# Kernel tuning notes

Measured on AMD Instinct MI355X. Metric: run time of the kernel, lower is better.

The kernel has to match this reference:

```python
import jax, jax.numpy as jnp
import numpy as np

DIM = 768
NUM_HEADS = 12
HEAD_DIM = DIM // NUM_HEADS
SCALE = HEAD_DIM ** -0.5


def setup_inputs() -> dict:
    key = jax.random.key(0)
    ks = jax.random.split(key, 6)
    B, N, C = 4, 2048, DIM
    x = jax.random.normal(ks[0], (B, N, C), dtype=jnp.float32)
    qkv_weight = jax.random.normal(ks[1], (3 * C, C), dtype=jnp.float32) * (C ** -0.5)
    q_bias = jax.random.normal(ks[2], (C,), dtype=jnp.float32) * 0.02
    v_bias = jax.random.normal(ks[3], (C,), dtype=jnp.float32) * 0.02
    proj_weight = jax.random.normal(ks[4], (C, C), dtype=jnp.float32) * (C ** -0.5)
    proj_bias = jax.random.normal(ks[5], (C,), dtype=jnp.float32) * 0.02
    return {"x": x, "qkv_weight": qkv_weight, "q_bias": q_bias,
            "v_bias": v_bias, "proj_weight": proj_weight, "proj_bias": proj_bias}


def reference(x, qkv_weight, q_bias, v_bias, proj_weight, proj_bias):
    B, N, C = x.shape
    # bias = concat(q_bias, zeros_like(v_bias), v_bias)
    bias = jnp.concatenate([q_bias, jnp.zeros_like(v_bias), v_bias])
    qkv = x @ qkv_weight.T + bias                      # [B, N, 3C]
    qkv = qkv.reshape(B, N, 3, NUM_HEADS, HEAD_DIM)
    q, k, v = jnp.moveaxis(qkv, 2, 0)                  # each [B, N, H, hd]
    q = jnp.transpose(q, (0, 2, 1, 3)) * SCALE         # [B, H, N, hd]
    k = jnp.transpose(k, (0, 2, 1, 3))
    v = jnp.transpose(v, (0, 2, 1, 3))
    attn = jax.nn.softmax(jnp.einsum('bhqd,bhkd->bhqk', q, k), axis=-1)
    out = jnp.einsum('bhqk,bhkd->bhqd', attn, v)       # [B, H, N, hd]
    out = jnp.transpose(out, (0, 2, 1, 3)).reshape(B, N, C)
    return out @ proj_weight.T + proj_bias
```

## Files before the change

### kernel.cpp

```cpp
#include <hip/hip_runtime.h>
#include <cstdint>
#include <cstddef>

typedef _Float16 f16;
typedef _Float16 f16x8 __attribute__((ext_vector_type(8)));
typedef _Float16 f16x4 __attribute__((ext_vector_type(4)));
typedef __fp16 h16x2 __attribute__((ext_vector_type(2)));
typedef float f32x4 __attribute__((ext_vector_type(4)));
typedef float f32x16 __attribute__((ext_vector_type(16)));

#define DIM 768
#define NHEAD 12
#define HD 64
#define BATCH 4
#define SEQ 2048
#define MROWS (BATCH*SEQ)
#define C3 (3*DIM)
#define NBH (BATCH*NHEAD)

__device__ __forceinline__ f32x4 mfma32(f16x8 a, f16x8 b, f32x4 c) {
  return __builtin_amdgcn_mfma_f32_16x16x32_f16(a, b, c, 0, 0, 0);
}
__device__ __forceinline__ f32x16 mfma3232(f16x8 a, f16x8 b, f32x16 c) {
  return __builtin_amdgcn_mfma_f32_32x32x16_f16(a, b, c, 0, 0, 0);
}

__device__ __forceinline__ void gl2lds16(const void* g, void* l) {
  __builtin_amdgcn_global_load_lds(
      (const __attribute__((address_space(1))) void*)g,
      (__attribute__((address_space(3))) void*)l, 16, 0, 0);
}

__global__ __launch_bounds__(256) void k_convert(
    const float* __restrict__ x, const float* __restrict__ wqkv,
    const float* __restrict__ wproj,
    f16* __restrict__ xh, f16* __restrict__ wqh, f16* __restrict__ wph)
{
  const int NX = MROWS*DIM/4, NW = C3*DIM/4;
  int i = blockIdx.x * 256 + threadIdx.x;
  const float4* src; f16* dst; int idx;
  if (i < NX)         { src = (const float4*)x;     dst = xh;  idx = i; }
  else if (i < NX+NW) { src = (const float4*)wqkv;  dst = wqh; idx = i - NX; }
  else                { src = (const float4*)wproj; dst = wph; idx = i - NX - NW; }
  float4 v = src[idx];
  union { f16 h[4]; uint64_t u; } r;
  r.h[0] = (f16)v.x; r.h[1] = (f16)v.y; r.h[2] = (f16)v.z; r.h[3] = (f16)v.w;
  ((uint64_t*)dst)[idx] = r.u;
}

__device__ __forceinline__ void gemm_tile(
    const f16* __restrict__ A, const f16* __restrict__ B,
    int lda, int ldb, int K, int am0, int bn0,
    f16* smem, f32x4 acc[4][4])
{
  f16* sA0 = smem;         f16* sA1 = smem + 4096;
  f16* sB0 = smem + 8192;  f16* sB1 = smem + 12288;
  const int tid = threadIdx.x, wid = tid >> 6;
  const int lane = tid & 63, lane15 = lane & 15, quad = lane >> 4;
  const int wm = wid >> 1, wn = wid & 1;

  auto stage = [&](int k0, f16* sA, f16* sB) {
    #pragma unroll
    for (int i = 0; i < 2; i++) {
      int j = i*256 + tid;
      int row = j >> 2;
      int sc  = (j & 3) ^ ((row >> 1) & 3);
      gl2lds16(A + (size_t)(am0 + row)*lda + k0 + sc*8, sA + (i*256 + wid*64)*8);
      gl2lds16(B + (size_t)(bn0 + row)*ldb + k0 + sc*8, sB + (i*256 + wid*64)*8);
    }
  };

  const int NK = K >> 5;
  stage(0, sA0, sB0);
  for (int kk = 0; kk < NK; kk++) {
    f16* cA = (kk & 1) ? sA1 : sA0;
    f16* cB = (kk & 1) ? sB1 : sB0;
    __syncthreads();
    if (kk + 1 < NK)
      stage((kk + 1) << 5, (kk & 1) ? sA0 : sA1, (kk & 1) ? sB0 : sB1);
    f16x8 af[4], bf[4];
    #pragma unroll
    for (int t = 0; t < 4; t++) {
      int ra = wm*64 + t*16 + lane15;
      af[t] = *(const f16x8*)(cA + ra*32 + ((quad ^ ((ra >> 1) & 3)) << 3));
      int rb = wn*64 + t*16 + lane15;
      bf[t] = *(const f16x8*)(cB + rb*32 + ((quad ^ ((rb >> 1) & 3)) << 3));
    }
    #pragma unroll
    for (int mt = 0; mt < 4; mt++)
      #pragma unroll
      for (int nt = 0; nt < 4; nt++)
        acc[mt][nt] = mfma32(af[mt], bf[nt], acc[mt][nt]);
  }
}

__global__ __launch_bounds__(256, 4) void k_qkv(
    const f16* __restrict__ xh, const f16* __restrict__ wqh,
    const float* __restrict__ q_bias, const float* __restrict__ v_bias,
    f16* __restrict__ Qh, f16* __restrict__ Kh, f16* __restrict__ Vt)
{
  __shared__ f16 smem[16384];
  f32x4 acc[4][4];
  const f32x4 z4 = {0.f, 0.f, 0.f, 0.f};
  #pragma unroll
  for (int a = 0; a < 4; a++)
    #pragma unroll
    for (int b = 0; b < 4; b++) acc[a][b] = z4;

  const int tid = threadIdx.x, wid = tid >> 6, lane = tid & 63;
  const int lane15 = lane & 15, quad = lane >> 4;
  const int wm = wid >> 1, wn = wid & 1;
  const int cblk = blockIdx.x * 128;
  const int mblk = blockIdx.y * 128;
  const int bb = mblk >> 11, nbase = mblk & (SEQ - 1);
  const float QS = 0.125f * 1.4426950408889634f;

  if (cblk < 2*DIM) {
    gemm_tile(wqh, xh, DIM, DIM, DIM, cblk, mblk, smem, acc);
    const bool isQ = (cblk < DIM);
    #pragma unroll
    for (int mt = 0; mt < 4; mt++) {
      int c0 = cblk + wm*64 + mt*16 + quad*4;
      int cr = isQ ? c0 : (c0 - DIM);
      int h = cr >> 6, d0 = cr & 63;
      float4 qb4 = isQ ? *(const float4*)(q_bias + c0) : make_float4(0,0,0,0);
      f16* dst = isQ ? Qh : Kh;
      f16* base = dst + (((size_t)(bb*NHEAD + h)*SEQ + nbase) << 6) + d0;
      #pragma unroll
      for (int nt = 0; nt < 4; nt++) {
        int n = wn*64 + nt*16 + lane15;
        f32x4 v = acc[mt][nt];
        f16x4 hv;
        if (isQ) {
          hv[0] = (f16)((v[0] + qb4.x) * QS); hv[1] = (f16)((v[1] + qb4.y) * QS);
          hv[2] = (f16)((v[2] + qb4.z) * QS); hv[3] = (f16)((v[3] + qb4.w) * QS);
        } else {
          hv[0] = (f16)v[0]; hv[1] = (f16)v[1]; hv[2] = (f16)v[2]; hv[3] = (f16)v[3];
        }
        *(f16x4*)(base + ((size_t)n << 6)) = hv;
      }
    }
  } else {
    gemm_tile(xh, wqh, DIM, DIM, DIM, mblk, cblk, smem, acc);
    #pragma unroll
    for (int nt = 0; nt < 4; nt++) {
      int c = cblk + wn*64 + nt*16 + lane15;
      int c2 = c - 2*DIM;
      int h = c2 >> 6, d = c2 & 63;
      float b = v_bias[c2];
      f16* base = Vt + ((size_t)(bb*NHEAD + h)*HD + d)*SEQ + nbase;
      #pragma unroll
      for (int mt = 0; mt < 4; mt++) {
        int n0 = wm*64 + mt*16 + quad*4;
        f32x4 v = acc[mt][nt];
        f16x4 hv = {(f16)(v[0]+b), (f16)(v[1]+b), (f16)(v[2]+b), (f16)(v[3]+b)};
        *(f16x4*)(base + n0) = hv;
      }
    }
  }
}

#define KVT 128
#define NIT (SEQ/KVT)
__global__ __launch_bounds__(256, 3) void k_attn(
    const f16* __restrict__ Qh, const f16* __restrict__ Kh,
    const f16* __restrict__ Vt, f16* __restrict__ attnh)
{
  __shared__ f16 smem[16384];
  f16* sK0 = smem;
  f16* sK1 = smem + 8192;

  const int tid = threadIdx.x, wid = tid >> 6, lane = tid & 63;
  const int l31 = lane & 31, hi = lane >> 5;

  const int L = blockIdx.x;
  const int xcd = L & 7, kk = L >> 3;
  const int bh = xcd + 8*(kk >> 4);
  const int q0 = (kk & 15) * 128;
  const int qw = q0 + wid*32;

  const f16* Kbh = Kh + (size_t)bh*SEQ*HD;
  const f16* Vbh = Vt + (size_t)bh*HD*SEQ;

  f16x8 qf[4];
  #pragma unroll
  for (int ks = 0; ks < 4; ks++)
    qf[ks] = *(const f16x8*)(Qh + ((size_t)bh*SEQ + qw + l31)*HD + ks*16 + hi*8);

  const f32x16 z16 = {0.f,0.f,0.f,0.f, 0.f,0.f,0.f,0.f,
                      0.f,0.f,0.f,0.f, 0.f,0.f,0.f,0.f};
  f32x16 o0 = z16, o1 = z16, sacc = z16;
  f16x8 one8;
  #pragma unroll
  for (int j = 0; j < 8; j++) one8[j] = (f16)1.f;

  auto stageK = [&](int kv0, f16* sK) {
    #pragma unroll
    for (int i = 0; i < 4; i++) {
      int j = i*256 + tid;
      int row = j >> 3;
      int sc  = (j & 7) ^ (row & 7);
      gl2lds16(Kbh + (size_t)(kv0 + row)*HD + sc*8, sK + (i*256 + wid*64)*8);
    }
  };

  int koff[4];
  #pragma unroll
  for (int ks = 0; ks < 4; ks++)
    koff[ks] = l31*64 + (((2*ks + hi) ^ (l31 & 7)) << 3);

  const f16* vb0 = Vbh + (size_t)l31*SEQ + hi*8;
  const f16* vb1 = Vbh + (size_t)(32 + l31)*SEQ + hi*8;

  const int pidx = (lane ^ 32) << 2;

  stageK(0, sK0);

  for (int it = 0; it < NIT; it++) {
    f16* cK = (it & 1) ? sK1 : sK0;
    __syncthreads();
    if (it + 1 < NIT)
      stageK((it + 1)*KVT, (it & 1) ? sK0 : sK1);

    #pragma unroll
    for (int c = 0; c < 4; c++) {
      const int p = it*KVT + c*32;
      f16x8 va00 = *(const f16x8*)(vb0 + p);
      f16x8 va01 = *(const f16x8*)(vb0 + p + 16);
      f16x8 va10 = *(const f16x8*)(vb1 + p);
      f16x8 va11 = *(const f16x8*)(vb1 + p + 16);

      f32x16 s = z16;
      #pragma unroll
      for (int ks = 0; ks < 4; ks++) {
        f16x8 ka = *(const f16x8*)(cK + c*2048 + koff[ks]);
        s = mfma3232(ka, qf[ks], s);
      }

      unsigned h[8];
      #pragma unroll
      for (int r = 0; r < 8; r++) {
        union { h16x2 p2; unsigned u; } uu;
        uu.p2 = __builtin_amdgcn_cvt_pkrtz(exp2f(s[2*r]), exp2f(s[2*r+1]));
        h[r] = uu.u;
      }
      int X0 = __builtin_amdgcn_ds_bpermute(pidx, (int)h[0]);
      int X1 = __builtin_amdgcn_ds_bpermute(pidx, (int)h[1]);
      int X2 = __builtin_amdgcn_ds_bpermute(pidx, (int)h[2]);
      int X3 = __builtin_amdgcn_ds_bpermute(pidx, (int)h[3]);
      int X4 = __builtin_amdgcn_ds_bpermute(pidx, (int)h[4]);
      int X5 = __builtin_amdgcn_ds_bpermute(pidx, (int)h[5]);
      int X6 = __builtin_amdgcn_ds_bpermute(pidx, (int)h[6]);
      int X7 = __builtin_amdgcn_ds_bpermute(pidx, (int)h[7]);
      union { unsigned w[4]; f16x8 v; } b0u, b1u;
      b0u.w[0] = hi ? (unsigned)X2 : h[0];
      b0u.w[1] = hi ? (unsigned)X3 : h[1];
      b0u.w[2] = hi ? h[2] : (unsigned)X0;
      b0u.w[3] = hi ? h[3] : (unsigned)X1;
      b1u.w[0] = hi ? (unsigned)X6 : h[4];
      b1u.w[1] = hi ? (unsigned)X7 : h[5];
      b1u.w[2] = hi ? h[6] : (unsigned)X4;
      b1u.w[3] = hi ? h[7] : (unsigned)X5;

      sacc = mfma3232(one8, b0u.v, sacc);
      sacc = mfma3232(one8, b1u.v, sacc);
      o0 = mfma3232(va00, b0u.v, o0);
      o0 = mfma3232(va01, b1u.v, o0);
      o1 = mfma3232(va10, b0u.v, o1);
      o1 = mfma3232(va11, b1u.v, o1);
    }
  }

  const float inv = 1.f / sacc[0];

  __syncthreads();
  f16* tb = smem + wid * (32 * 72);
  #pragma unroll
  for (int g = 0; g < 4; g++) {
    f16x4 h0v = {(f16)(o0[4*g+0]*inv), (f16)(o0[4*g+1]*inv),
                 (f16)(o0[4*g+2]*inv), (f16)(o0[4*g+3]*inv)};
    *(f16x4*)(tb + l31*72 + g*8 + hi*4) = h0v;
    f16x4 h1v = {(f16)(o1[4*g+0]*inv), (f16)(o1[4*g+1]*inv),
                 (f16)(o1[4*g+2]*inv), (f16)(o1[4*g+3]*inv)};
    *(f16x4*)(tb + l31*72 + 32 + g*8 + hi*4) = h1v;
  }
  __syncthreads();
  const int b = bh / NHEAD, hh = bh % NHEAD;
  #pragma unroll
  for (int i = 0; i < 4; i++) {
    int row = i*8 + (lane >> 3);
    f16x8 rv = *(const f16x8*)(tb + row*72 + (lane & 7)*8);
    *(f16x8*)(attnh + ((size_t)b*SEQ + qw + row)*DIM + hh*HD + (lane & 7)*8) = rv;
  }
}

__global__ __launch_bounds__(256, 4) void k_proj(
    const f16* __restrict__ ah, const f16* __restrict__ wph,
    const float* __restrict__ pbias, float* __restrict__ out)
{
  __shared__ f16 smem[16384];
  f32x4 acc[4][4];
  const f32x4 z4 = {0.f, 0.f, 0.f, 0.f};
  #pragma unroll
  for (int a = 0; a < 4; a++)
    #pragma unroll
    for (int b = 0; b < 4; b++) acc[a][b] = z4;

  const int cblk = blockIdx.y * 128;
  const int mblk = blockIdx.x * 128;
  gemm_tile(wph, ah, DIM, DIM, DIM, cblk, mblk, smem, acc);

  const int tid = threadIdx.x, wid = tid >> 6, lane = tid & 63;
  const int lane15 = lane & 15, quad = lane >> 4;
  const int wm = wid >> 1, wn = wid & 1;
  #pragma unroll
  for (int mt = 0; mt < 4; mt++) {
    int c0 = cblk + wm*64 + mt*16 + quad*4;
    float4 b4 = *(const float4*)(pbias + c0);
    #pragma unroll
    for (int nt = 0; nt < 4; nt++) {
      int m = mblk + wn*64 + nt*16 + lane15;
      f32x4 v = acc[mt][nt];
      float4 r = make_float4(v[0]+b4.x, v[1]+b4.y, v[2]+b4.z, v[3]+b4.w);
      *(float4*)(out + (size_t)m*DIM + c0) = r;
    }
  }
}

extern "C" void kernel_launch(void* const* d_in, const int* in_sizes, int n_in,
                              void* d_out, int out_size, void* d_ws, size_t ws_size,
                              hipStream_t stream) {
  const float* x    = (const float*)d_in[0];
  const float* wqkv = (const float*)d_in[1];
  const float* qb   = (const float*)d_in[2];
  const float* vb   = (const float*)d_in[3];
  const float* wp   = (const float*)d_in[4];
  const float* pb   = (const float*)d_in[5];
  float* out = (float*)d_out;

  f16* p = (f16*)d_ws;
  f16* xh  = p; p += (size_t)MROWS*DIM;
  f16* wqh = p; p += (size_t)C3*DIM;
  f16* wph = p; p += (size_t)DIM*DIM;
  f16* Qh  = p; p += (size_t)NBH*SEQ*HD;
  f16* Kh  = p; p += (size_t)NBH*SEQ*HD;
  f16* Vt  = p; p += (size_t)NBH*SEQ*HD;
  f16* attnh = xh;

  k_convert<<<8448, 256, 0, stream>>>(x, wqkv, wp, xh, wqh, wph);
  k_qkv<<<dim3(C3/128, MROWS/128), 256, 0, stream>>>(xh, wqh, qb, vb, Qh, Kh, Vt);
  k_attn<<<dim3((SEQ/128)*NBH), 256, 0, stream>>>(Qh, Kh, Vt, attnh);
  k_proj<<<dim3(MROWS/128, DIM/128), 256, 0, stream>>>(attnh, wph, pb, out);
}
```

Before: 251.0 us.

## Permute V loads to match score layout and prefetch V one chunk ahead

Drops the ds_bpermute exchange of exponentiated scores by loading V in a column order (4-element pieces offset by 4*hi) that matches the MFMA accumulator layout directly. V fragments are now double-buffered in registers and the next chunk is loaded while the current one computes, to hide global load latency. exp2f is also replaced by the hardware exp2 builtin. The cost is more register pressure from two V buffers and smaller 8-byte loads instead of 16-byte ones.

Result: slower. 330.9 us (+31.8%).

```diff
diff --git a/kernel.cpp b/kernel.cpp
--- a/kernel.cpp
+++ b/kernel.cpp
@@ -209,11 +209,55 @@
   for (int ks = 0; ks < 4; ks++)
     koff[ks] = l31*64 + (((2*ks + hi) ^ (l31 & 7)) << 3);
 
-  const f16* vb0 = Vbh + (size_t)l31*SEQ + hi*8;
-  const f16* vb1 = Vbh + (size_t)(32 + l31)*SEQ + hi*8;
-
-  const int pidx = (lane ^ 32) << 2;
-
+  const f16* vb0 = Vbh + (size_t)l31*SEQ + 4*hi;
+  const f16* vb1 = Vbh + (size_t)(32 + l31)*SEQ + 4*hi;
+
+  f16x4 vA[8], vB[8];
+  auto loadV = [&](int p, f16x4* vr) {
+    vr[0] = *(const f16x4*)(vb0 + p);
+    vr[1] = *(const f16x4*)(vb0 + p + 8);
+    vr[2] = *(const f16x4*)(vb0 + p + 16);
+    vr[3] = *(const f16x4*)(vb0 + p + 24);
+    vr[4] = *(const f16x4*)(vb1 + p);
+    vr[5] = *(const f16x4*)(vb1 + p + 8);
+    vr[6] = *(const f16x4*)(vb1 + p + 16);
+    vr[7] = *(const f16x4*)(vb1 + p + 24);
+  };
+
+#define CHUNK(VCUR, VNXT, coff, PRE)                                          \
+  do {                                                                        \
+    PRE;                                                                      \
+    f32x16 s = z16;                                                           \
+    _Pragma("unroll")                                                         \
+    for (int ks = 0; ks < 4; ks++) {                                          \
+      f16x8 ka = *(const f16x8*)(cK + (coff)*2048 + koff[ks]);                \
+      s = mfma3232(ka, qf[ks], s);                                            \
+    }                                                                         \
+    unsigned h[8];                                                            \
+    _Pragma("unroll")                                                         \
+    for (int r = 0; r < 8; r++) {                                             \
+      union { h16x2 p2; unsigned u; } uu;                                     \
+      uu.p2 = __builtin_amdgcn_cvt_pkrtz(__builtin_amdgcn_exp2f(s[2*r]),      \
+                                         __builtin_amdgcn_exp2f(s[2*r+1]));   \
+      h[r] = uu.u;                                                            \
+    }                                                                         \
+    union { unsigned w[4]; f16x8 v; } b0u, b1u;                               \
+    b0u.w[0]=h[0]; b0u.w[1]=h[1]; b0u.w[2]=h[2]; b0u.w[3]=h[3];               \
+    b1u.w[0]=h[4]; b1u.w[1]=h[5]; b1u.w[2]=h[6]; b1u.w[3]=h[7];               \
+    union { f16x4 q[2]; f16x8 v; } a00, a01, a10, a11;                        \
+    a00.q[0]=VCUR[0]; a00.q[1]=VCUR[1];                                       \
+    a01.q[0]=VCUR[2]; a01.q[1]=VCUR[3];                                       \
+    a10.q[0]=VCUR[4]; a10.q[1]=VCUR[5];                                       \
+    a11.q[0]=VCUR[6]; a11.q[1]=VCUR[7];                                       \
+    sacc = mfma3232(one8, b0u.v, sacc);                                       \
+    sacc = mfma3232(one8, b1u.v, sacc);                                       \
+    o0 = mfma3232(a00.v, b0u.v, o0);                                          \
+    o0 = mfma3232(a01.v, b1u.v, o0);                                          \
+    o1 = mfma3232(a10.v, b0u.v, o1);                                          \
+    o1 = mfma3232(a11.v, b1u.v, o1);                                          \
+  } while (0)
+
+  loadV(0, vA);
   stageK(0, sK0);
 
   for (int it = 0; it < NIT; it++) {
@@ -221,55 +265,13 @@
     __syncthreads();
     if (it + 1 < NIT)
       stageK((it + 1)*KVT, (it & 1) ? sK0 : sK1);
-
-    #pragma unroll
-    for (int c = 0; c < 4; c++) {
-      const int p = it*KVT + c*32;
-      f16x8 va00 = *(const f16x8*)(vb0 + p);
-      f16x8 va01 = *(const f16x8*)(vb0 + p + 16);
-      f16x8 va10 = *(const f16x8*)(vb1 + p);
-      f16x8 va11 = *(const f16x8*)(vb1 + p + 16);
-
-      f32x16 s = z16;
-      #pragma unroll
-      for (int ks = 0; ks < 4; ks++) {
-        f16x8 ka = *(const f16x8*)(cK + c*2048 + koff[ks]);
-        s = mfma3232(ka, qf[ks], s);
-      }
-
-      unsigned h[8];
-      #pragma unroll
-      for (int r = 0; r < 8; r++) {
-        union { h16x2 p2; unsigned u; } uu;
-        uu.p2 = __builtin_amdgcn_cvt_pkrtz(exp2f(s[2*r]), exp2f(s[2*r+1]));
-        h[r] = uu.u;
-      }
-      int X0 = __builtin_amdgcn_ds_bpermute(pidx, (int)h[0]);
-      int X1 = __builtin_amdgcn_ds_bpermute(pidx, (int)h[1]);
-      int X2 = __builtin_amdgcn_ds_bpermute(pidx, (int)h[2]);
-      int X3 = __builtin_amdgcn_ds_bpermute(pidx, (int)h[3]);
-      int X4 = __builtin_amdgcn_ds_bpermute(pidx, (int)h[4]);
-      int X5 = __builtin_amdgcn_ds_bpermute(pidx, (int)h[5]);
-      int X6 = __builtin_amdgcn_ds_bpermute(pidx, (int)h[6]);
-      int X7 = __builtin_amdgcn_ds_bpermute(pidx, (int)h[7]);
-      union { unsigned w[4]; f16x8 v; } b0u, b1u;
-      b0u.w[0] = hi ? (unsigned)X2 : h[0];
-      b0u.w[1] = hi ? (unsigned)X3 : h[1];
-      b0u.w[2] = hi ? h[2] : (unsigned)X0;
-      b0u.w[3] = hi ? h[3] : (unsigned)X1;
-      b1u.w[0] = hi ? (unsigned)X6 : h[4];
-      b1u.w[1] = hi ? (unsigned)X7 : h[5];
-      b1u.w[2] = hi ? h[6] : (unsigned)X4;
-      b1u.w[3] = hi ? h[7] : (unsigned)X5;
-
-      sacc = mfma3232(one8, b0u.v, sacc);
-      sacc = mfma3232(one8, b1u.v, sacc);
-      o0 = mfma3232(va00, b0u.v, o0);
-      o0 = mfma3232(va01, b1u.v, o0);
-      o1 = mfma3232(va10, b0u.v, o1);
-      o1 = mfma3232(va11, b1u.v, o1);
-    }
-  }
+    const int p0 = it*KVT;
+    CHUNK(vA, vB, 0, loadV(p0 + 32, vB));
+    CHUNK(vB, vA, 1, loadV(p0 + 64, vA));
+    CHUNK(vA, vB, 2, loadV(p0 + 96, vB));
+    CHUNK(vB, vA, 3, if (it + 1 < NIT) loadV(p0 + 128, vA));
+  }
+#undef CHUNK
 
   const float inv = 1.f / sacc[0];
 
```

## Stage V tiles through padded LDS and drop bpermute P-fragment shuffle

Applied to the files above, without the earlier changes.

V tiles are now prefetched into registers one iteration ahead and written into a padded shared-memory buffer. Each wave then reads the V fragments from LDS in an order that matches the MFMA output layout of the exp'd scores, which removes the eight ds_bpermute cross-lane shuffles per chunk. The exp2 call is replaced by the hardware exp2 builtin. The cost is an extra barrier per iteration, about 17KB more LDS per block, which may lower occupancy from the launch-bounds target of 3 blocks, and more LDS traffic.

Result: faster. 220.1 us (-12.3%).

```diff
diff --git a/kernel.cpp b/kernel.cpp
--- a/kernel.cpp
+++ b/kernel.cpp
@@ -166,9 +166,10 @@
     const f16* __restrict__ Qh, const f16* __restrict__ Kh,
     const f16* __restrict__ Vt, f16* __restrict__ attnh)
 {
-  __shared__ f16 smem[16384];
+  __shared__ f16 smem[2*8192 + 64*132];
   f16* sK0 = smem;
   f16* sK1 = smem + 8192;
+  f16* sV  = smem + 16384;
 
   const int tid = threadIdx.x, wid = tid >> 6, lane = tid & 63;
   const int l31 = lane & 31, hi = lane >> 5;
@@ -209,26 +210,43 @@
   for (int ks = 0; ks < 4; ks++)
     koff[ks] = l31*64 + (((2*ks + hi) ^ (l31 & 7)) << 3);
 
-  const f16* vb0 = Vbh + (size_t)l31*SEQ + hi*8;
-  const f16* vb1 = Vbh + (size_t)(32 + l31)*SEQ + hi*8;
-
-  const int pidx = (lane ^ 32) << 2;
+  const int vrow = tid >> 2, vcg = (tid & 3) * 32;
+  const f16* vsrc = Vbh + (size_t)vrow*SEQ + vcg;
 
   stageK(0, sK0);
+  f16x8 vreg[4];
+  #pragma unroll
+  for (int j = 0; j < 4; j++) vreg[j] = *(const f16x8*)(vsrc + j*8);
 
   for (int it = 0; it < NIT; it++) {
     f16* cK = (it & 1) ? sK1 : sK0;
     __syncthreads();
-    if (it + 1 < NIT)
+    #pragma unroll
+    for (int j = 0; j < 4; j++) {
+      union { f16x8 v; f16x4 h[2]; } u; u.v = vreg[j];
+      *(f16x4*)(sV + vrow*132 + vcg + j*8)     = u.h[0];
+      *(f16x4*)(sV + vrow*132 + vcg + j*8 + 4) = u.h[1];
+    }
+    __syncthreads();
+    if (it + 1 < NIT) {
       stageK((it + 1)*KVT, (it & 1) ? sK0 : sK1);
+      #pragma unroll
+      for (int j = 0; j < 4; j++)
+        vreg[j] = *(const f16x8*)(vsrc + (it + 1)*KVT + j*8);
+    }
 
     #pragma unroll
     for (int c = 0; c < 4; c++) {
-      const int p = it*KVT + c*32;
-      f16x8 va00 = *(const f16x8*)(vb0 + p);
-      f16x8 va01 = *(const f16x8*)(vb0 + p + 16);
-      f16x8 va10 = *(const f16x8*)(vb1 + p);
-      f16x8 va11 = *(const f16x8*)(vb1 + p + 16);
+      const int vo = c*32 + 4*hi;
+      union { f16x4 q[2]; f16x8 v; } a00, a01, a10, a11;
+      a00.q[0] = *(const f16x4*)(sV + l31*132 + vo);
+      a00.q[1] = *(const f16x4*)(sV + l31*132 + vo + 8);
+      a01.q[0] = *(const f16x4*)(sV + l31*132 + vo + 16);
+      a01.q[1] = *(const f16x4*)(sV + l31*132 + vo + 24);
+      a10.q[0] = *(const f16x4*)(sV + (32 + l31)*132 + vo);
+      a10.q[1] = *(const f16x4*)(sV + (32 + l31)*132 + vo + 8);
+      a11.q[0] = *(const f16x4*)(sV + (32 + l31)*132 + vo + 16);
+      a11.q[1] = *(const f16x4*)(sV + (32 + l31)*132 + vo + 24);
 
       f32x16 s = z16;
       #pragma unroll
@@ -241,33 +259,20 @@
       #pragma unroll
       for (int r = 0; r < 8; r++) {
         union { h16x2 p2; unsigned u; } uu;
-        uu.p2 = __builtin_amdgcn_cvt_pkrtz(exp2f(s[2*r]), exp2f(s[2*r+1]));
+        uu.p2 = __builtin_amdgcn_cvt_pkrtz(__builtin_amdgcn_exp2f(s[2*r]),
+                                           __builtin_amdgcn_exp2f(s[2*r+1]));
         h[r] = uu.u;
       }
-      int X0 = __builtin_amdgcn_ds_bpermute(pidx, (int)h[0]);
-      int X1 = __builtin_amdgcn_ds_bpermute(pidx, (int)h[1]);
-      int X2 = __builtin_amdgcn_ds_bpermute(pidx, (int)h[2]);
-      int X3 = __builtin_amdgcn_ds_bpermute(pidx, (int)h[3]);
-      int X4 = __builtin_amdgcn_ds_bpermute(pidx, (int)h[4]);
-      int X5 = __builtin_amdgcn_ds_bpermute(pidx, (int)h[5]);
-      int X6 = __builtin_amdgcn_ds_bpermute(pidx, (int)h[6]);
-      int X7 = __builtin_amdgcn_ds_bpermute(pidx, (int)h[7]);
       union { unsigned w[4]; f16x8 v; } b0u, b1u;
-      b0u.w[0] = hi ? (unsigned)X2 : h[0];
-      b0u.w[1] = hi ? (unsigned)X3 : h[1];
-      b0u.w[2] = hi ? h[2] : (unsigned)X0;
-      b0u.w[3] = hi ? h[3] : (unsigned)X1;
-      b1u.w[0] = hi ? (unsigned)X6 : h[4];
-      b1u.w[1] = hi ? (unsigned)X7 : h[5];
-      b1u.w[2] = hi ? h[6] : (unsigned)X4;
-      b1u.w[3] = hi ? h[7] : (unsigned)X5;
+      b0u.w[0]=h[0]; b0u.w[1]=h[1]; b0u.w[2]=h[2]; b0u.w[3]=h[3];
+      b1u.w[0]=h[4]; b1u.w[1]=h[5]; b1u.w[2]=h[6]; b1u.w[3]=h[7];
 
       sacc = mfma3232(one8, b0u.v, sacc);
       sacc = mfma3232(one8, b1u.v, sacc);
-      o0 = mfma3232(va00, b0u.v, o0);
-      o0 = mfma3232(va01, b1u.v, o0);
-      o1 = mfma3232(va10, b0u.v, o1);
-      o1 = mfma3232(va11, b1u.v, o1);
+      o0 = mfma3232(a00.v, b0u.v, o0);
+      o0 = mfma3232(a01.v, b1u.v, o0);
+      o1 = mfma3232(a10.v, b0u.v, o1);
+      o1 = mfma3232(a11.v, b1u.v, o1);
     }
   }
 
```
